# Performance work log

Hardware: AMD Instinct MI355X
Metric: run time of the kernel (lower is better)

The kernel has to match this reference:

```python
import jax, jax.numpy as jnp
import numpy as np

HEADS = 4
DIM_HEAD = 32
SCALE = DIM_HEAD ** -0.5

# Energy conventions (Hopfield / Lagrangian formulation):
#  Neuron(x): g = activation(x); e = sum(x*g) - L(x)
#  Synapse(g, x): e = -sum(g*x)
#  identity Lagrangian: L(x) = 0.5*sum(x^2), g = x  => Conv2d block energy = -0.5*sum(x^2)
#  softmax Lagrangian: L(x) = sum(logsumexp(x, -1)), g = softmax(x, -1)

def setup_inputs() -> dict:
    key = jax.random.key(0)
    ks = jax.random.split(key, 5)
    b, c, h, w = 8, 256, 48, 48
    hidden = HEADS * DIM_HEAD  # 128
    return {
        "x": jax.random.normal(ks[0], (b, c, h, w), jnp.float32),
        "w_qkv": jax.random.normal(ks[1], (hidden * 3, c), jnp.float32) * 0.02,
        "b_qkv": jax.random.normal(ks[2], (hidden * 3,), jnp.float32) * 0.02,
        "w_out": jax.random.normal(ks[3], (c, hidden), jnp.float32) * 0.02,
        "b_out": jax.random.normal(ks[4], (c,), jnp.float32) * 0.02,
    }

def reference(x, w_qkv, b_qkv, w_out, b_out):
    b, c, h, w = x.shape
    # 1x1 conv == channel matmul
    qkv = jnp.einsum('oc,bcxy->boxy', w_qkv, x) + b_qkv[None, :, None, None]
    e_qkv = -0.5 * jnp.sum(qkv * qkv)  # identity-Lagrangian neuron + synapse energy
    q, k, v = jnp.split(qkv, 3, axis=1)
    # 'b (h c) x y -> b h c (x y)'
    def heads(t):
        return t.reshape(b, HEADS, DIM_HEAD, h * w)
    q, k, v = heads(q), heads(k), heads(v)
    q = q * SCALE
    sim = jnp.einsum('bhdi,bhdj->bhij', q, k)  # [b, heads, hw, hw]
    sim = sim - jax.lax.stop_gradient(jnp.max(sim, axis=-1, keepdims=True))
    attn = jax.nn.softmax(sim, axis=-1)
    # softmax-Lagrangian neuron energy: sum(sim*attn) - sum(logsumexp(sim, -1))
    e_attn = jnp.sum(sim * attn) - jnp.sum(jax.nn.logsumexp(sim, axis=-1))
    out = jnp.einsum('bhij,bhdj->bhid', attn, v)  # [b, heads, hw, dim_head]
    # 'b h (x y) d -> b (h d) x y'
    out = out.transpose(0, 1, 3, 2).reshape(b, HEADS * DIM_HEAD, h, w)
    out = jnp.einsum('oc,bcxy->boxy', w_out, out) + b_out[None, :, None, None]
    e_out = -0.5 * jnp.sum(out * out)
    return out, e_attn + e_out + e_qkv
```

## Files before the change

### kernel.cpp

```cpp
#include <hip/hip_runtime.h>
#include <hip/hip_bf16.h>

#define HW 2304
#define HW2 4608
#define NB 8
#define NC 256
#define HID 128
#define DH 32
#define NH 4
#define SCALE 0.17677669529663687f
#define LOG2E 1.4426950408889634f
#define LN2   0.6931471805599453f

#define NSPLIT 4
#define OSZ ((size_t)NB * HW * HID)

using bf16x8 = __attribute__((ext_vector_type(8))) short;
using f32x4  = __attribute__((ext_vector_type(4))) float;

__device__ __forceinline__ short f2bf(float f) {
    unsigned u = __float_as_uint(f);
    u += 0x7FFF + ((u >> 16) & 1);
    return (short)(u >> 16);
}
__device__ __forceinline__ float bf2f(short s) {
    return __uint_as_float(((unsigned)(unsigned short)s) << 16);
}
__device__ __forceinline__ unsigned pk2bf(float a, float b) {
    union { __hip_bfloat162 h; unsigned u; } cv;
    cv.h = __float22bfloat162_rn(float2{a, b});
    return cv.u;
}
__device__ __forceinline__ void gld16(const void* g, void* l) {
    __builtin_amdgcn_global_load_lds(
        (const __attribute__((address_space(1))) unsigned*)g,
        (__attribute__((address_space(3))) unsigned*)l, 16, 0, 0);
}
#define SB() __builtin_amdgcn_sched_barrier(0)

__global__ __launch_bounds__(256)
void prep(const float* __restrict__ x, const float* __restrict__ wq,
          const float* __restrict__ wo, short* __restrict__ Xt,
          short* __restrict__ Wq, short* __restrict__ Wo, float* __restrict__ wsz)
{
    if (blockIdx.z == 8) {
        const int bid = blockIdx.x + 36 * blockIdx.y;
        if (bid == 0 && threadIdx.x == 0) { wsz[0] = 0.f; ((int*)wsz)[1] = 0; }
        for (int i = bid * 256 + threadIdx.x; i < 384 * 256; i += 144 * 256) {
            Wq[i] = f2bf(wq[i]);
            if (i < 256 * 128) Wo[i] = f2bf(wo[i]);
        }
        return;
    }
    __shared__ short Tb[64][72];
    const int b = blockIdx.z, c0 = blockIdx.y * 64, s0 = blockIdx.x * 64;
    const int ts4 = (threadIdx.x & 15) * 4;
    const int cc0 = threadIdx.x >> 4;
    #pragma unroll
    for (int pp = 0; pp < 4; ++pp) {
        const int cc = cc0 + pp * 16;
        const float4 v = *(const float4*)(
            x + ((size_t)b * NC + c0 + cc) * HW + s0 + ts4);
        Tb[ts4 + 0][cc] = f2bf(v.x);
        Tb[ts4 + 1][cc] = f2bf(v.y);
        Tb[ts4 + 2][cc] = f2bf(v.z);
        Tb[ts4 + 3][cc] = f2bf(v.w);
    }
    __syncthreads();
    const int ss = threadIdx.x >> 2;
    const int c8 = (threadIdx.x & 3) * 8;
    #pragma unroll
    for (int pp = 0; pp < 2; ++pp) {
        const int cc = c8 + pp * 32;
        const bf16x8 v = *(const bf16x8*)&Tb[ss][cc];
        *(bf16x8*)(Xt + ((size_t)b * HW + s0 + ss) * NC + c0 + cc) = v;
    }
}

__global__ __launch_bounds__(256, 2)
void conv_qkv(const short* __restrict__ A, const short* __restrict__ Bt,
              const float* __restrict__ bias,
              short* __restrict__ Qb, short* __restrict__ Kb,
              short* __restrict__ Kt, short* __restrict__ Vb,
              float* __restrict__ E)
{
    constexpr int KD = NC;
    constexpr int NI = KD / 64;
    const int flat = blockIdx.x + 18 * (blockIdx.y + 6 * blockIdx.z);
    const int xcd  = flat & 7, j = flat >> 3;
    const int g    = xcd + 8 * (j / 6);
    const int b    = g / 18;
    const int bn   = (g % 18) * 128;
    const int bm   = (j % 6) * 64;
    const int t  = threadIdx.x;
    const int w  = t >> 6, lane = t & 63;
    const int n16 = lane & 15, quad = lane >> 4;

    __shared__ __align__(16) char csm[2 * 24576];
    __shared__ float red[4];

    const int rL = lane >> 2, cswz = (lane & 3) ^ (rL & 3);
    const char* agl = (const char*)(A  + (size_t)(bm + rL) * KD + cswz * 8);
    const char* bgl = (const char*)(Bt + ((size_t)b * HW + bn + rL) * KD + cswz * 8);

    auto issue32 = [&](int kc, char* base) {
        if (w == 0) {
            gld16(agl + (size_t)(0 * 16 * KD + kc) * 2, base + 0 * 1024);
            gld16(agl + (size_t)(1 * 16 * KD + kc) * 2, base + 1 * 1024);
            gld16(bgl + (size_t)(0 * 16 * KD + kc) * 2, base + 4096 + 0 * 1024);
        } else if (w == 1) {
            gld16(agl + (size_t)(2 * 16 * KD + kc) * 2, base + 2 * 1024);
            gld16(agl + (size_t)(3 * 16 * KD + kc) * 2, base + 3 * 1024);
            gld16(bgl + (size_t)(1 * 16 * KD + kc) * 2, base + 4096 + 1 * 1024);
        } else if (w == 2) {
            gld16(bgl + (size_t)(2 * 16 * KD + kc) * 2, base + 4096 + 2 * 1024);
            gld16(bgl + (size_t)(3 * 16 * KD + kc) * 2, base + 4096 + 3 * 1024);
            gld16(bgl + (size_t)(4 * 16 * KD + kc) * 2, base + 4096 + 4 * 1024);
        } else {
            gld16(bgl + (size_t)(5 * 16 * KD + kc) * 2, base + 4096 + 5 * 1024);
            gld16(bgl + (size_t)(6 * 16 * KD + kc) * 2, base + 4096 + 6 * 1024);
            gld16(bgl + (size_t)(7 * 16 * KD + kc) * 2, base + 4096 + 7 * 1024);
        }
    };
    auto stage = [&](int kc, int pbuf) {
        issue32(kc,      csm + pbuf * 24576);
        issue32(kc + 32, csm + pbuf * 24576 + 12288);
    };

    f32x4 acc[4][2] = {};
    const int rsw = (quad ^ (n16 & 3)) * 16;

    stage(0, 0); SB();
    for (int ki = 0; ki < NI; ++ki) {
        const int p = ki & 1;
        asm volatile("s_waitcnt vmcnt(0)" ::: "memory");
        __builtin_amdgcn_s_barrier();
        SB();
        if (ki + 1 < NI) stage((ki + 1) * 64, p ^ 1);

        #pragma unroll
        for (int su = 0; su < 2; ++su) {
            const char* Ap = csm + p * 24576 + su * 12288;
            const char* Bp = Ap + 4096;
            bf16x8 am[4], bq[2];
            #pragma unroll
            for (int tm = 0; tm < 4; ++tm)
                am[tm] = *(const bf16x8*)(Ap + tm * 1024 + n16 * 64 + rsw);
            #pragma unroll
            for (int j2 = 0; j2 < 2; ++j2)
                bq[j2] = *(const bf16x8*)(Bp + (w * 2 + j2) * 1024 + n16 * 64 + rsw);
            #pragma unroll
            for (int tm = 0; tm < 4; ++tm)
                #pragma unroll
                for (int j2 = 0; j2 < 2; ++j2)
                    acc[tm][j2] = __builtin_amdgcn_mfma_f32_16x16x32_bf16(am[tm], bq[j2], acc[tm][j2], 0, 0, 0);
        }
    }

    float e = 0.f;
    #pragma unroll
    for (int tm = 0; tm < 4; ++tm) {
        const int o0 = bm + tm * 16 + quad * 4;
        const float4 bb = *(const float4*)(bias + o0);
        #pragma unroll
        for (int j2 = 0; j2 < 2; ++j2) {
            const int s = bn + (w * 2 + j2) * 16 + n16;
            float v[4] = {acc[tm][j2][0] + bb.x, acc[tm][j2][1] + bb.y,
                          acc[tm][j2][2] + bb.z, acc[tm][j2][3] + bb.w};
            e -= 0.5f * (v[0]*v[0] + v[1]*v[1] + v[2]*v[2] + v[3]*v[3]);
            if (o0 < HID) {
                const int h = o0 >> 5, dh0 = o0 & 31;
                const float qs = SCALE * LOG2E;
                short4 pk = {f2bf(v[0]*qs), f2bf(v[1]*qs),
                             f2bf(v[2]*qs), f2bf(v[3]*qs)};
                *(short4*)(Qb + ((size_t)(b * NH + h) * HW + s) * DH + dh0) = pk;
            } else if (o0 < 2 * HID) {
                const int c = o0 - HID, h = c >> 5, dh0 = c & 31;
                const int gg = s & 31;
                const int sp = (s & ~31) | ((gg & 4) << 2) | ((gg >> 3) << 2) | (gg & 3);
                short4 pk = {f2bf(v[0]), f2bf(v[1]), f2bf(v[2]), f2bf(v[3])};
                *(short4*)(Kb + ((size_t)(b * NH + h) * HW + sp) * DH + dh0) = pk;
                #pragma unroll
                for (int r = 0; r < 4; ++r)
                    Kt[((size_t)(b * NH + h) * DH + dh0 + r) * HW + s] = f2bf(v[r]);
            } else {
                const int c = o0 - 2 * HID, h = c >> 5, dh0 = c & 31;
                #pragma unroll
                for (int r = 0; r < 4; ++r)
                    Vb[((size_t)(b * NH + h) * DH + dh0 + r) * HW + s] = f2bf(v[r]);
            }
        }
    }

    #pragma unroll
    for (int off = 32; off > 0; off >>= 1) e += __shfl_down(e, off);
    if (lane == 0) red[w] = e;
    __syncthreads();
    if (t == 0) atomicAdd(E, red[0] + red[1] + red[2] + red[3]);
}

__global__ __launch_bounds__(256)
void flashsplit(const short* __restrict__ Qb, const short* __restrict__ Kb,
                const short* __restrict__ Kt, const short* __restrict__ Vb,
                short* __restrict__ Oh, float* __restrict__ lsP,
                float* __restrict__ tsP)
{
    __shared__ __align__(16) char smem[2 * 12288];

    constexpr int ITERS = HW / (NSPLIT * 64);
    const int flat = blockIdx.x + 18 * (blockIdx.y + 32 * blockIdx.z);
    const int xcd  = flat & 7, j = flat >> 3;
    const int g    = xcd + 8 * (j / 18);
    const int m    = j % 18;
    const int bh   = g & 31;
    const int kh   = g >> 5;
    const int w    = threadIdx.x >> 6;
    const int lane = threadIdx.x & 63;
    const int n16  = lane & 15, quad = lane >> 4;
    const int qb   = m * 128 + w * 32;
    const int key0 = kh * ITERS * 64;

    bf16x8 aq[2];
    #pragma unroll
    for (int qg = 0; qg < 2; ++qg)
        aq[qg] = *(const bf16x8*)(Qb + ((size_t)bh * HW + qb + qg * 16 + n16) * DH + quad * 8);
    SB();

    const int rL = lane >> 2, cL = (lane & 3) ^ (rL & 3);
    const char* Kglb  = (const char*)(Kb + (size_t)bh * HW * DH);
    const char* Vglb  = (const char*)(Vb + (size_t)bh * DH * HW);
    const char* Ktglb = (const char*)(Kt + (size_t)bh * DH * HW);
    const int pca  = w & 1;
    const int ktca = w >> 1;
    const int ktu  = w & 1;

    auto stage = [&](int it, int pbuf) {
        char* buf = smem + pbuf * 12288;
        const int k64 = key0 + it * 64;
        if (w < 2) {
            const char* kg = Kglb + (size_t)(k64 + pca * 32 + rL) * 64 + cL * 16;
            gld16(kg,        buf + pca * 6144 + 0);
            gld16(kg + 1024, buf + pca * 6144 + 1024);
        } else {
            const char* vg = Vglb + (size_t)rL * HW2 + (size_t)(k64 + pca * 32) * 2 + cL * 16;
            gld16(vg,             buf + pca * 6144 + 2048);
            gld16(vg + 16 * HW2,  buf + pca * 6144 + 3072);
        }
        const char* kt = Ktglb + (size_t)(ktu * 16 + rL) * HW2
                       + (size_t)(k64 + ktca * 32) * 2 + cL * 16;
        gld16(kt, buf + ktca * 6144 + 4096 + ktu * 1024);
    };

    stage(0, 0);
    SB();

    f32x4 acc[2][2] = {};
    f32x4 lsacc[2] = {};
    f32x4 tsacc[2][2] = {};
    const int swz = (quad ^ (n16 & 3)) * 8;
    const bf16x8 ones = {0x3F80, 0x3F80, 0x3F80, 0x3F80,
                         0x3F80, 0x3F80, 0x3F80, 0x3F80};

    for (int it = 0; it < ITERS; ++it) {
        const int p = it & 1;
        asm volatile("s_waitcnt vmcnt(0)" ::: "memory");
        __builtin_amdgcn_s_barrier();
        SB();
        if (it + 1 < ITERS) stage(it + 1, p ^ 1);

        const char* buf = smem + p * 12288;
        #pragma unroll
        for (int ca = 0; ca < 2; ++ca) {
            const short* cb = (const short*)(buf + ca * 6144);

            const bf16x8 bk0  = *(const bf16x8*)(cb +        n16 * 32 + swz);
            const bf16x8 bk1  = *(const bf16x8*)(cb + 512  + n16 * 32 + swz);
            const bf16x8 bv0  = *(const bf16x8*)(cb + 1024 + n16 * 32 + swz);
            const bf16x8 bv1  = *(const bf16x8*)(cb + 1536 + n16 * 32 + swz);
            const bf16x8 bkt0 = *(const bf16x8*)(cb + 2048 + n16 * 32 + swz);
            const bf16x8 bkt1 = *(const bf16x8*)(cb + 2560 + n16 * 32 + swz);

            #pragma unroll
            for (int qg = 0; qg < 2; ++qg) {
                f32x4 z = {};
                const f32x4 s0 = __builtin_amdgcn_mfma_f32_16x16x32_bf16(bk0, aq[qg], z, 0, 0, 0);
                const f32x4 s1 = __builtin_amdgcn_mfma_f32_16x16x32_bf16(bk1, aq[qg], z, 0, 0, 0);
                float e0[4], e1[4];
                #pragma unroll
                for (int r = 0; r < 4; ++r) {
                    e0[r] = __builtin_amdgcn_exp2f(s0[r]);
                    e1[r] = __builtin_amdgcn_exp2f(s1[r]);
                }
                union { bf16x8 v; unsigned u[4]; } pa;
                pa.u[0] = pk2bf(e0[0], e0[1]);
                pa.u[1] = pk2bf(e0[2], e0[3]);
                pa.u[2] = pk2bf(e1[0], e1[1]);
                pa.u[3] = pk2bf(e1[2], e1[3]);
                acc[qg][0]   = __builtin_amdgcn_mfma_f32_16x16x32_bf16(bv0,  pa.v, acc[qg][0], 0, 0, 0);
                acc[qg][1]   = __builtin_amdgcn_mfma_f32_16x16x32_bf16(bv1,  pa.v, acc[qg][1], 0, 0, 0);
                lsacc[qg]    = __builtin_amdgcn_mfma_f32_16x16x32_bf16(ones, pa.v, lsacc[qg], 0, 0, 0);
                tsacc[qg][0] = __builtin_amdgcn_mfma_f32_16x16x32_bf16(bkt0, pa.v, tsacc[qg][0], 0, 0, 0);
                tsacc[qg][1] = __builtin_amdgcn_mfma_f32_16x16x32_bf16(bkt1, pa.v, tsacc[qg][1], 0, 0, 0);
            }
        }
    }

    const int bb = bh >> 2, h = bh & 3;
    short* dst = Oh + (size_t)kh * OSZ;
    #pragma unroll
    for (int qg = 0; qg < 2; ++qg) {
        const int q = qb + qg * 16 + n16;
        const float L = lsacc[qg][0];
        const short4 qa = *(const short4*)(Qb + ((size_t)bh * HW + q) * DH + quad * 4);
        const short4 qc = *(const short4*)(Qb + ((size_t)bh * HW + q) * DH + 16 + quad * 4);
        float ts = bf2f(qa.x) * tsacc[qg][0][0] + bf2f(qa.y) * tsacc[qg][0][1]
                 + bf2f(qa.z) * tsacc[qg][0][2] + bf2f(qa.w) * tsacc[qg][0][3]
                 + bf2f(qc.x) * tsacc[qg][1][0] + bf2f(qc.y) * tsacc[qg][1][1]
                 + bf2f(qc.z) * tsacc[qg][1][2] + bf2f(qc.w) * tsacc[qg][1][3];
        ts += __shfl_xor(ts, 16);
        ts += __shfl_xor(ts, 32);

        const float invl = 1.f / L;
        short* ap = dst + ((size_t)bb * HW + q) * HID + h * 32;
        short4 pk0 = {f2bf(acc[qg][0][0] * invl), f2bf(acc[qg][0][1] * invl),
                      f2bf(acc[qg][0][2] * invl), f2bf(acc[qg][0][3] * invl)};
        short4 pk1 = {f2bf(acc[qg][1][0] * invl), f2bf(acc[qg][1][1] * invl),
                      f2bf(acc[qg][1][2] * invl), f2bf(acc[qg][1][3] * invl)};
        *(short4*)(ap + quad * 4)      = pk0;
        *(short4*)(ap + 16 + quad * 4) = pk1;
        if (quad == 0) {
            const size_t li = (size_t)(kh * 32 + bh) * HW + q;
            lsP[li] = L;
            tsP[li] = ts;
        }
    }
}

__global__ __launch_bounds__(256, 2)
void conv_out(const short* __restrict__ A, const short* __restrict__ Oh,
              const float* __restrict__ lsP, const float* __restrict__ tsP,
              const float* __restrict__ bias, float* __restrict__ out0,
              float* __restrict__ E, int* __restrict__ ticket, int nblocks,
              float* __restrict__ edst)
{
    constexpr int KD = HID;
    constexpr int NI = KD / 32;
    const int flat = blockIdx.x + 18 * (blockIdx.y + 4 * blockIdx.z);
    const int xcd  = flat & 7, j = flat >> 3;
    const int g    = xcd + 8 * (j / 4);
    const int b    = g / 18;
    const int bn   = (g % 18) * 128;
    const int bmi  = j % 4;
    const int bm   = bmi * 64;
    const int t  = threadIdx.x;
    const int w  = t >> 6, lane = t & 63;
    const int n16 = lane & 15, quad = lane >> 4;

    __shared__ __align__(16) char csm[24576];
    __shared__ float red[4];

    const int rL = lane >> 2, cswz = (lane & 3) ^ (rL & 3);
    const char* agl = (const char*)(A + (size_t)(bm + rL) * KD + cswz * 8);

    auto issueA = [&](int kc, int pbuf) {
        char* base = csm + pbuf * 12288;
        if (w == 0) {
            gld16(agl + (size_t)(0 * 16 * KD + kc) * 2, base + 0 * 1024);
            gld16(agl + (size_t)(1 * 16 * KD + kc) * 2, base + 1 * 1024);
        } else if (w == 1) {
            gld16(agl + (size_t)(2 * 16 * KD + kc) * 2, base + 2 * 1024);
            gld16(agl + (size_t)(3 * 16 * KD + kc) * 2, base + 3 * 1024);
        }
    };

    auto loadB = [&](int ki, bf16x8 pk[2]) {
        const int kc = ki * 32;
        const int bh = b * NH + ki;
        #pragma unroll
        for (int d = 0; d < 2; ++d) {
            const int blk = w * 2 + d;
            const int q = bn + blk * 16 + rL;
            float Ls[NSPLIT], sum = 0.f;
            #pragma unroll
            for (int kh = 0; kh < NSPLIT; ++kh) {
                Ls[kh] = lsP[(size_t)(kh * 32 + bh) * HW + q];
                sum += Ls[kh];
            }
            const float inv = 1.f / sum;
            float vv[8] = {};
            #pragma unroll
            for (int kh = 0; kh < NSPLIT; ++kh) {
                const float wk = Ls[kh] * inv;
                const bf16x8 o = *(const bf16x8*)(Oh + (size_t)kh * OSZ
                                    + ((size_t)b * HW + q) * HID + kc + cswz * 8);
                #pragma unroll
                for (int jj = 0; jj < 8; ++jj) vv[jj] += wk * bf2f(o[jj]);
            }
            union { bf16x8 v; unsigned u[4]; } c;
            #pragma unroll
            for (int i = 0; i < 4; ++i) c.u[i] = pk2bf(vv[2*i], vv[2*i+1]);
            pk[d] = c.v;
        }
    };
    auto writeB = [&](const bf16x8 pk[2], int pbuf) {
        char* base = csm + pbuf * 12288 + 4096;
        #pragma unroll
        for (int d = 0; d < 2; ++d) {
            const int blk = w * 2 + d;
            *(bf16x8*)(base + blk * 1024 + rL * 64 + (lane & 3) * 16) = pk[d];
        }
    };

    f32x4 acc[4][2] = {};
    const int rsw = (quad ^ (n16 & 3)) * 16;

    bf16x8 bpk[2];
    loadB(0, bpk);
    issueA(0, 0);
    writeB(bpk, 0);
    for (int ki = 0; ki < NI; ++ki) {
        const int p = ki & 1;
        __syncthreads();
        if (ki + 1 < NI) { loadB(ki + 1, bpk); issueA((ki + 1) * 32, p ^ 1); }

        const char* Ap = csm + p * 12288;
        const char* Bp = Ap + 4096;
        bf16x8 am[4], bq[2];
        #pragma unroll
        for (int tm = 0; tm < 4; ++tm)
            am[tm] = *(const bf16x8*)(Ap + tm * 1024 + n16 * 64 + rsw);
        #pragma unroll
        for (int jj = 0; jj < 2; ++jj)
            bq[jj] = *(const bf16x8*)(Bp + (w * 2 + jj) * 1024 + n16 * 64 + rsw);
        #pragma unroll
        for (int tm = 0; tm < 4; ++tm)
            #pragma unroll
            for (int jj = 0; jj < 2; ++jj)
                acc[tm][jj] = __builtin_amdgcn_mfma_f32_16x16x32_bf16(am[tm], bq[jj], acc[tm][jj], 0, 0, 0);

        if (ki + 1 < NI) writeB(bpk, p ^ 1);
    }

    float e = 0.f;
    #pragma unroll
    for (int tm = 0; tm < 4; ++tm) {
        const int o0 = bm + tm * 16 + quad * 4;
        const float4 bb = *(const float4*)(bias + o0);
        #pragma unroll
        for (int jj = 0; jj < 2; ++jj) {
            const int s = bn + (w * 2 + jj) * 16 + n16;
            float v[4] = {acc[tm][jj][0] + bb.x, acc[tm][jj][1] + bb.y,
                          acc[tm][jj][2] + bb.z, acc[tm][jj][3] + bb.w};
            e -= 0.5f * (v[0]*v[0] + v[1]*v[1] + v[2]*v[2] + v[3]*v[3]);
            #pragma unroll
            for (int r = 0; r < 4; ++r)
                out0[((size_t)b * NC + o0 + r) * HW + s] = v[r];
        }
    }

    if (bmi == 0) {
        const int q = bn + (t & 127);
        #pragma unroll
        for (int jj = 0; jj < 2; ++jj) {
            const int h = (t >> 7) * 2 + jj;
            const int bh = b * NH + h;
            float L = 0.f, T = 0.f;
            #pragma unroll
            for (int kh = 0; kh < NSPLIT; ++kh) {
                L += lsP[(size_t)(kh * 32 + bh) * HW + q];
                T += tsP[(size_t)(kh * 32 + bh) * HW + q];
            }
            e += (LN2 * T) / L - __logf(L);
        }
    }

    #pragma unroll
    for (int off = 32; off > 0; off >>= 1) e += __shfl_down(e, off);
    if (lane == 0) red[w] = e;
    __syncthreads();
    if (t == 0) {
        atomicAdd(E, red[0] + red[1] + red[2] + red[3]);
        __threadfence();
        const int prev = atomicAdd(ticket, 1);
        if (prev == nblocks - 1) {
            __threadfence();
            edst[0] = atomicAdd(E, 0.f);
        }
    }
}

extern "C" void kernel_launch(void* const* d_in, const int* in_sizes, int n_in,
                              void* d_out, int out_size, void* d_ws, size_t ws_size,
                              hipStream_t stream) {
    const float* x     = (const float*)d_in[0];
    const float* w_qkv = (const float*)d_in[1];
    const float* b_qkv = (const float*)d_in[2];
    const float* w_out = (const float*)d_in[3];
    const float* b_out = (const float*)d_in[4];
    float* out = (float*)d_out;

    float* wsf    = (float*)d_ws;
    float* E      = wsf;
    int*   ticket = (int*)d_ws + 1;
    short* Xt   = (short*)(wsf + 16);
    short* Wq   = Xt + (size_t)NB * HW * NC;
    short* Wo   = Wq + 384 * 256;
    short* Qb   = Wo + 256 * 128;
    short* Kb   = Qb + (size_t)NB * NH * HW * DH;
    short* Ktb  = Kb + (size_t)NB * NH * HW * DH;
    short* Vb   = Ktb + (size_t)NB * NH * HW * DH;
    short* Oh   = Vb + (size_t)NB * NH * HW * DH;
    float* lsP  = (float*)(Oh + NSPLIT * OSZ);
    float* tsP  = lsP + NSPLIT * 32 * HW;

    prep<<<dim3(HW / 64, NC / 64, NB + 1), 256, 0, stream>>>(
        x, w_qkv, w_out, Xt, Wq, Wo, wsf);
    conv_qkv<<<dim3(18, 6, NB), 256, 0, stream>>>(
        Wq, Xt, b_qkv, Qb, Kb, Ktb, Vb, E);
    flashsplit<<<dim3(HW / 128, NB * NH, NSPLIT), 256, 0, stream>>>(
        Qb, Kb, Ktb, Vb, Oh, lsP, tsP);
    conv_out<<<dim3(18, 4, NB), 256, 0, stream>>>(
        Wo, Oh, lsP, tsP, b_out, out, E, ticket, 18 * 4 * NB,
        out + (size_t)NB * NC * HW);
}
```

Measured before the change: 181.8 us.

## Compute softmax row sums and entropy terms on VALU instead of extra MFMAs

The flash kernel used to accumulate the row sum with an MFMA against a ones vector and the sum(p*s) term with MFMAs against a transposed K copy, then dotted that with Q at the end. Both are now accumulated directly from the exponentials and scores in registers, followed by cross-lane shuffles. This drops three of the five MFMAs per step, the Kt staging loads and LDS space, and the Kt writes in conv_qkv, which also raises its occupancy hint to 3. The cost is extra VALU multiply-adds in the inner loop and a different fp32 summation order.

```diff
diff --git a/kernel.cpp b/kernel.cpp
--- a/kernel.cpp
+++ b/kernel.cpp
@@ -77,12 +77,11 @@
     }
 }
 
-__global__ __launch_bounds__(256, 2)
+__global__ __launch_bounds__(256, 3)
 void conv_qkv(const short* __restrict__ A, const short* __restrict__ Bt,
               const float* __restrict__ bias,
               short* __restrict__ Qb, short* __restrict__ Kb,
-              short* __restrict__ Kt, short* __restrict__ Vb,
-              float* __restrict__ E)
+              short* __restrict__ Vb, float* __restrict__ E)
 {
     constexpr int KD = NC;
     constexpr int NI = KD / 64;
@@ -180,9 +179,6 @@
                 const int sp = (s & ~31) | ((gg & 4) << 2) | ((gg >> 3) << 2) | (gg & 3);
                 short4 pk = {f2bf(v[0]), f2bf(v[1]), f2bf(v[2]), f2bf(v[3])};
                 *(short4*)(Kb + ((size_t)(b * NH + h) * HW + sp) * DH + dh0) = pk;
-                #pragma unroll
-                for (int r = 0; r < 4; ++r)
-                    Kt[((size_t)(b * NH + h) * DH + dh0 + r) * HW + s] = f2bf(v[r]);
             } else {
                 const int c = o0 - 2 * HID, h = c >> 5, dh0 = c & 31;
                 #pragma unroll
@@ -201,11 +197,10 @@
 
 __global__ __launch_bounds__(256)
 void flashsplit(const short* __restrict__ Qb, const short* __restrict__ Kb,
-                const short* __restrict__ Kt, const short* __restrict__ Vb,
-                short* __restrict__ Oh, float* __restrict__ lsP,
-                float* __restrict__ tsP)
+                const short* __restrict__ Vb, short* __restrict__ Oh,
+                float* __restrict__ lsP, float* __restrict__ tsP)
 {
-    __shared__ __align__(16) char smem[2 * 12288];
+    __shared__ __align__(16) char smem[2 * 8192];
 
     constexpr int ITERS = HW / (NSPLIT * 64);
     const int flat = blockIdx.x + 18 * (blockIdx.y + 32 * blockIdx.z);
@@ -227,39 +222,30 @@
     SB();
 
     const int rL = lane >> 2, cL = (lane & 3) ^ (rL & 3);
-    const char* Kglb  = (const char*)(Kb + (size_t)bh * HW * DH);
-    const char* Vglb  = (const char*)(Vb + (size_t)bh * DH * HW);
-    const char* Ktglb = (const char*)(Kt + (size_t)bh * DH * HW);
-    const int pca  = w & 1;
-    const int ktca = w >> 1;
-    const int ktu  = w & 1;
+    const char* Kglb = (const char*)(Kb + (size_t)bh * HW * DH);
+    const char* Vglb = (const char*)(Vb + (size_t)bh * DH * HW);
+    const int pca = w & 1;
 
     auto stage = [&](int it, int pbuf) {
-        char* buf = smem + pbuf * 12288;
+        char* buf = smem + pbuf * 8192;
         const int k64 = key0 + it * 64;
         if (w < 2) {
             const char* kg = Kglb + (size_t)(k64 + pca * 32 + rL) * 64 + cL * 16;
-            gld16(kg,        buf + pca * 6144 + 0);
-            gld16(kg + 1024, buf + pca * 6144 + 1024);
+            gld16(kg,        buf + pca * 4096 + 0);
+            gld16(kg + 1024, buf + pca * 4096 + 1024);
         } else {
             const char* vg = Vglb + (size_t)rL * HW2 + (size_t)(k64 + pca * 32) * 2 + cL * 16;
-            gld16(vg,             buf + pca * 6144 + 2048);
-            gld16(vg + 16 * HW2,  buf + pca * 6144 + 3072);
-        }
-        const char* kt = Ktglb + (size_t)(ktu * 16 + rL) * HW2
-                       + (size_t)(k64 + ktca * 32) * 2 + cL * 16;
-        gld16(kt, buf + ktca * 6144 + 4096 + ktu * 1024);
+            gld16(vg,            buf + pca * 4096 + 2048);
+            gld16(vg + 16 * HW2, buf + pca * 4096 + 3072);
+        }
     };
 
     stage(0, 0);
     SB();
 
     f32x4 acc[2][2] = {};
-    f32x4 lsacc[2] = {};
-    f32x4 tsacc[2][2] = {};
+    float ls[2] = {}, ts[2] = {};
     const int swz = (quad ^ (n16 & 3)) * 8;
-    const bf16x8 ones = {0x3F80, 0x3F80, 0x3F80, 0x3F80,
-                         0x3F80, 0x3F80, 0x3F80, 0x3F80};
 
     for (int it = 0; it < ITERS; ++it) {
         const int p = it & 1;
@@ -268,17 +254,15 @@
         SB();
         if (it + 1 < ITERS) stage(it + 1, p ^ 1);
 
-        const char* buf = smem + p * 12288;
+        const char* buf = smem + p * 8192;
         #pragma unroll
         for (int ca = 0; ca < 2; ++ca) {
-            const short* cb = (const short*)(buf + ca * 6144);
-
-            const bf16x8 bk0  = *(const bf16x8*)(cb +        n16 * 32 + swz);
-            const bf16x8 bk1  = *(const bf16x8*)(cb + 512  + n16 * 32 + swz);
-            const bf16x8 bv0  = *(const bf16x8*)(cb + 1024 + n16 * 32 + swz);
-            const bf16x8 bv1  = *(const bf16x8*)(cb + 1536 + n16 * 32 + swz);
-            const bf16x8 bkt0 = *(const bf16x8*)(cb + 2048 + n16 * 32 + swz);
-            const bf16x8 bkt1 = *(const bf16x8*)(cb + 2560 + n16 * 32 + swz);
+            const short* cb = (const short*)(buf + ca * 4096);
+
+            const bf16x8 bk0 = *(const bf16x8*)(cb +        n16 * 32 + swz);
+            const bf16x8 bk1 = *(const bf16x8*)(cb + 512  + n16 * 32 + swz);
+            const bf16x8 bv0 = *(const bf16x8*)(cb + 1024 + n16 * 32 + swz);
+            const bf16x8 bv1 = *(const bf16x8*)(cb + 1536 + n16 * 32 + swz);
 
             #pragma unroll
             for (int qg = 0; qg < 2; ++qg) {
@@ -291,18 +275,27 @@
                     e0[r] = __builtin_amdgcn_exp2f(s0[r]);
                     e1[r] = __builtin_amdgcn_exp2f(s1[r]);
                 }
+                ls[qg] += (e0[0] + e0[1]) + (e0[2] + e0[3])
+                        + (e1[0] + e1[1]) + (e1[2] + e1[3]);
+                ts[qg] += (e0[0]*s0[0] + e0[1]*s0[1]) + (e0[2]*s0[2] + e0[3]*s0[3])
+                        + (e1[0]*s1[0] + e1[1]*s1[1]) + (e1[2]*s1[2] + e1[3]*s1[3]);
                 union { bf16x8 v; unsigned u[4]; } pa;
                 pa.u[0] = pk2bf(e0[0], e0[1]);
                 pa.u[1] = pk2bf(e0[2], e0[3]);
                 pa.u[2] = pk2bf(e1[0], e1[1]);
                 pa.u[3] = pk2bf(e1[2], e1[3]);
-                acc[qg][0]   = __builtin_amdgcn_mfma_f32_16x16x32_bf16(bv0,  pa.v, acc[qg][0], 0, 0, 0);
-                acc[qg][1]   = __builtin_amdgcn_mfma_f32_16x16x32_bf16(bv1,  pa.v, acc[qg][1], 0, 0, 0);
-                lsacc[qg]    = __builtin_amdgcn_mfma_f32_16x16x32_bf16(ones, pa.v, lsacc[qg], 0, 0, 0);
-                tsacc[qg][0] = __builtin_amdgcn_mfma_f32_16x16x32_bf16(bkt0, pa.v, tsacc[qg][0], 0, 0, 0);
-                tsacc[qg][1] = __builtin_amdgcn_mfma_f32_16x16x32_bf16(bkt1, pa.v, tsacc[qg][1], 0, 0, 0);
+                acc[qg][0] = __builtin_amdgcn_mfma_f32_16x16x32_bf16(bv0, pa.v, acc[qg][0], 0, 0, 0);
+                acc[qg][1] = __builtin_amdgcn_mfma_f32_16x16x32_bf16(bv1, pa.v, acc[qg][1], 0, 0, 0);
             }
         }
+    }
+
+    #pragma unroll
+    for (int qg = 0; qg < 2; ++qg) {
+        ls[qg] += __shfl_xor(ls[qg], 16);
+        ls[qg] += __shfl_xor(ls[qg], 32);
+        ts[qg] += __shfl_xor(ts[qg], 16);
+        ts[qg] += __shfl_xor(ts[qg], 32);
     }
 
     const int bb = bh >> 2, h = bh & 3;
@@ -310,16 +303,7 @@
     #pragma unroll
     for (int qg = 0; qg < 2; ++qg) {
         const int q = qb + qg * 16 + n16;
-        const float L = lsacc[qg][0];
-        const short4 qa = *(const short4*)(Qb + ((size_t)bh * HW + q) * DH + quad * 4);
-        const short4 qc = *(const short4*)(Qb + ((size_t)bh * HW + q) * DH + 16 + quad * 4);
-        float ts = bf2f(qa.x) * tsacc[qg][0][0] + bf2f(qa.y) * tsacc[qg][0][1]
-                 + bf2f(qa.z) * tsacc[qg][0][2] + bf2f(qa.w) * tsacc[qg][0][3]
-                 + bf2f(qc.x) * tsacc[qg][1][0] + bf2f(qc.y) * tsacc[qg][1][1]
-                 + bf2f(qc.z) * tsacc[qg][1][2] + bf2f(qc.w) * tsacc[qg][1][3];
-        ts += __shfl_xor(ts, 16);
-        ts += __shfl_xor(ts, 32);
-
+        const float L = ls[qg];
         const float invl = 1.f / L;
         short* ap = dst + ((size_t)bb * HW + q) * HID + h * 32;
         short4 pk0 = {f2bf(acc[qg][0][0] * invl), f2bf(acc[qg][0][1] * invl),
@@ -331,7 +315,7 @@
         if (quad == 0) {
             const size_t li = (size_t)(kh * 32 + bh) * HW + q;
             lsP[li] = L;
-            tsP[li] = ts;
+            tsP[li] = ts[qg];
         }
     }
 }
@@ -507,8 +491,7 @@
     short* Wo   = Wq + 384 * 256;
     short* Qb   = Wo + 256 * 128;
     short* Kb   = Qb + (size_t)NB * NH * HW * DH;
-    short* Ktb  = Kb + (size_t)NB * NH * HW * DH;
-    short* Vb   = Ktb + (size_t)NB * NH * HW * DH;
+    short* Vb   = Kb + (size_t)NB * NH * HW * DH;
     short* Oh   = Vb + (size_t)NB * NH * HW * DH;
     float* lsP  = (float*)(Oh + NSPLIT * OSZ);
     float* tsP  = lsP + NSPLIT * 32 * HW;
@@ -516,9 +499,9 @@
     prep<<<dim3(HW / 64, NC / 64, NB + 1), 256, 0, stream>>>(
         x, w_qkv, w_out, Xt, Wq, Wo, wsf);
     conv_qkv<<<dim3(18, 6, NB), 256, 0, stream>>>(
-        Wq, Xt, b_qkv, Qb, Kb, Ktb, Vb, E);
-    flashsplit<<<dim3(HW / 128, NB * NH, NSPLIT), 256, 0, stream>>>(
-        Qb, Kb, Ktb, Vb, Oh, lsP, tsP);
+        Wq, Xt, b_qkv, Qb, Kb, Vb, E);
+    flashsplit<<<dim3(18, 32, NSPLIT), 256, 0, stream>>>(
+        Qb, Kb, Vb, Oh, lsP, tsP);
     conv_out<<<dim3(18, 4, NB), 256, 0, stream>>>(
         Wo, Oh, lsP, tsP, b_out, out, E, ticket, 18 * 4 * NB,
         out + (size_t)NB * NC * HW);
```

New measurement: 182.0 us. No clear change (+0.1%).
